# Kernel optimization log

Hardware: AMD Instinct MI355X
Metric: run time of the kernel (lower is better)

Reference implementation:

```python
import jax, jax.numpy as jnp
import numpy as np

B, N, E = 2, 30000, 120000
IN_F, OUT_F, H = 512, 512, 4
D = OUT_F // H  # head_dim = 128
LN_EPS = 1e-5


def setup_inputs() -> dict:
    key = jax.random.key(0)
    k1, k2, k3, k4 = jax.random.split(key, 4)
    node_features = jax.random.normal(k1, (B, N, IN_F), dtype=jnp.float32)
    edge_index = jax.random.randint(k2, (2, E), 0, N, dtype=jnp.int64)
    # per-head linear transforms (bias=False): W[h] is [in_features, head_dim]
    W = jax.random.normal(k3, (H, IN_F, D), dtype=jnp.float32) / np.sqrt(IN_F)
    # per-head attention vectors a[h] is [2*head_dim] (Linear(2*head_dim,1,bias=False))
    a = jax.random.normal(k4, (H, 2 * D), dtype=jnp.float32) / np.sqrt(2 * D)
    ln_gamma = jnp.ones((OUT_F,), dtype=jnp.float32)
    ln_beta = jnp.zeros((OUT_F,), dtype=jnp.float32)
    return {"node_features": node_features, "edge_index": edge_index,
            "W": W, "a": a, "ln_gamma": ln_gamma, "ln_beta": ln_beta}


def reference(node_features, edge_index, W, a, ln_gamma, ln_beta):
    src, dst = edge_index[0], edge_index[1]
    # all-heads linear transform: [B, H, N, D]
    t = jnp.einsum('bni,hid->bhnd', node_features, W)
    # per-edge gathered features: [B, H, E, D]
    sf = t[:, :, src, :]
    df = t[:, :, dst, :]
    # attention score = [sf ; df] . a  == sf.a_src + df.a_dst  -> [B, H, E]
    scores = (jnp.einsum('bhed,hd->bhe', sf, a[:, :D])
              + jnp.einsum('bhed,hd->bhe', df, a[:, D:]))
    scores = jax.nn.leaky_relu(scores, negative_slope=0.2)
    # NOTE: faithful to source — softmax over ALL edges (dim=-1), not per-dst
    w = jax.nn.softmax(scores, axis=-1)
    # scatter-add aggregation into destination nodes (the Python-loop in torch)
    agg = jnp.zeros_like(t).at[:, :, dst, :].add(w[..., None] * sf)  # [B,H,N,D]
    # concat heads along feature dim (head order preserved)
    out = jnp.transpose(agg, (0, 2, 1, 3)).reshape(node_features.shape[0], N, H * D)
    # LayerNorm over last dim
    mu = jnp.mean(out, axis=-1, keepdims=True)
    var = jnp.mean(jnp.square(out - mu), axis=-1, keepdims=True)
    out = (out - mu) * jax.lax.rsqrt(var + LN_EPS) * ln_gamma + ln_beta
    return out
```

## Files before the change

kernel.cpp:

```cpp
#include <hip/hip_runtime.h>
#include <stdint.h>

#define Bn 2
#define Nn 30000
#define En 120000
#define KIN 512
#define Hh 4
#define Dd 128
#define MROWS 60000
#define MPAD  60032
#define LNEPS 1e-5f
#define EBLK 469

typedef unsigned short u16;
typedef unsigned int   u32;
typedef __attribute__((ext_vector_type(8))) short short8;
typedef __attribute__((ext_vector_type(4))) float f32x4;

__device__ __forceinline__ u16 f2bf(float f) {
    u32 u = __builtin_bit_cast(u32, f);
    u32 r = u + 0x7FFFu + ((u >> 16) & 1u);
    return (u16)(r >> 16);
}
__device__ __forceinline__ float bflo(u32 u) {
    return __builtin_bit_cast(float, u << 16);
}
__device__ __forceinline__ float bfhi(u32 u) {
    return __builtin_bit_cast(float, u & 0xFFFF0000u);
}
__device__ __forceinline__ void ld16(void* lds, const void* g) {
    __builtin_amdgcn_global_load_lds((const __attribute__((address_space(1))) void*)g,
                                     (__attribute__((address_space(3))) void*)lds, 16, 0, 0);
}

#define CVTW_BLKS 1024
__global__ void prep_kernel(const float* __restrict__ W, u16* __restrict__ wbt,
                            const int* __restrict__ ei, int* __restrict__ deg) {
    int blk = blockIdx.x;
    if (blk < CVTW_BLKS) {
        int idx = blk * 256 + threadIdx.x;
        int c = idx >> 9, i = idx & 511;
        int h = c >> 7, d = c & 127;
        wbt[idx] = f2bf(W[h * (KIN * Dd) + i * Dd + d]);
    } else {
        int e = (blk - CVTW_BLKS) * 256 + threadIdx.x;
        if (e < En) atomicAdd(&deg[ei[En + e]], 1);
    }
}

__device__ void scan512(const int* __restrict__ deg, int* __restrict__ offs,
                        int* __restrict__ cursor, int* __restrict__ part) {
    int tid = threadIdx.x;
    const int CH = 59;
    int start = tid * CH;
    int s = 0;
    for (int i = 0; i < CH; i++) {
        int n = start + i;
        if (n < Nn) s += deg[n];
    }
    part[tid] = s;
    __syncthreads();
    for (int off = 1; off < 512; off <<= 1) {
        int xv = (tid >= off) ? part[tid - off] : 0;
        __syncthreads();
        part[tid] += xv;
        __syncthreads();
    }
    int run = part[tid] - s;
    for (int i = 0; i < CH; i++) {
        int n = start + i;
        if (n < Nn) {
            offs[n] = run;
            cursor[n] = run;
            run += deg[n];
        }
    }
    if (tid == 511) offs[Nn] = part[511];
}

#define A_LDS (2 * 128 * 32)
#define B_LDS (2 * 512 * 32)
__launch_bounds__(512)
__global__ void gemm(const float* __restrict__ x, const u16* __restrict__ wbt,
                     const float* __restrict__ ag, u16* __restrict__ t,
                     float* __restrict__ s1g, float* __restrict__ s2g,
                     const int* __restrict__ deg, int* __restrict__ offs,
                     int* __restrict__ cursor) {
    __shared__ __align__(16) u16 smem[A_LDS + B_LDS];
    if (blockIdx.x == 0) { scan512(deg, offs, cursor, (int*)smem); return; }
    u16* As0 = smem;
    u16* As1 = smem + 128 * 32;
    u16* Bs0 = smem + A_LDS;
    u16* Bs1 = smem + A_LDS + 512 * 32;
    const int tid = threadIdx.x;
    const int m0 = (blockIdx.x - 1) * 128;
    const int w = tid >> 6, l = tid & 63;
    const int lr = l & 15, lk = l >> 4;
    const int wrM = (w >> 2) * 64;
    const int h = w & 3;
    const int wc = h * 128;
    const int swz = (lk * 8) ^ ((lr & 6) << 2);
    int aoff[4], boff[8];
    #pragma unroll
    for (int mi = 0; mi < 4; mi++) aoff[mi] = (wrM + mi * 16 + lr) * 32 + swz;
    #pragma unroll
    for (int nj = 0; nj < 8; nj++) boff[nj] = (wc + nj * 16 + lr) * 32 + swz;

    const int arow_u = m0 + (tid >> 2);
    const int arow = arow_u < MROWS ? arow_u : (MROWS - 1);
    const float* xsrc = x + (long)arow * KIN + (tid & 3) * 8;
    const int awr = (tid >> 2) * 32 + (((tid & 3) * 8) ^ (((tid >> 2) & 6) << 2));

    const int grow = tid >> 2, gslot = tid & 3;
    const int gsw = (gslot * 8) ^ ((grow & 6) << 2);
    const u16* bgsrc = wbt + (long)grow * KIN + gsw;
    f32x4 acc[4][8] = {};
    float4 a0A, a1A, a0B, a1B;

#define LOADX(R0, R1, KS)                                           \
    {                                                               \
        R0 = *(const float4*)(xsrc + (KS) * 32);                    \
        R1 = *(const float4*)(xsrc + (KS) * 32 + 4);                \
    }
#define CVTW(BUF, R0, R1)                                           \
    {                                                               \
        short8 o;                                                   \
        o[0] = (short)f2bf(R0.x); o[1] = (short)f2bf(R0.y);         \
        o[2] = (short)f2bf(R0.z); o[3] = (short)f2bf(R0.w);         \
        o[4] = (short)f2bf(R1.x); o[5] = (short)f2bf(R1.y);         \
        o[6] = (short)f2bf(R1.z); o[7] = (short)f2bf(R1.w);         \
        *(short8*)&(BUF)[awr] = o;                                  \
    }

    auto STAGEB = [&](u16* Bb, int k0) {
        #pragma unroll
        for (int i = 0; i < 4; i++)
            ld16(Bb + ((long)(i * 512 + tid)) * 8, bgsrc + (long)i * 128 * KIN + k0);
    };

    LOADX(a0A, a1A, 0);
    LOADX(a0B, a1B, 1);
    STAGEB(Bs0, 0);
    CVTW(As0, a0A, a1A);
    __syncthreads();

    #pragma unroll
    for (int t16 = 0; t16 < 16; t16++) {
        u16* Acur = (t16 & 1) ? As1 : As0;
        u16* Bcur = (t16 & 1) ? Bs1 : Bs0;
        u16* Anext = (t16 & 1) ? As0 : As1;
        u16* Bnext = (t16 & 1) ? Bs0 : Bs1;
        if (t16 < 14) {
            if (t16 & 1) { LOADX(a0B, a1B, t16 + 2); }
            else         { LOADX(a0A, a1A, t16 + 2); }
        }
        if (t16 < 15) STAGEB(Bnext, (t16 + 1) * 32);
        short8 af[4];
        #pragma unroll
        for (int mi = 0; mi < 4; mi++) af[mi] = *(const short8*)&Acur[aoff[mi]];
        #pragma unroll
        for (int nj = 0; nj < 8; nj++) {
            short8 bv = *(const short8*)&Bcur[boff[nj]];
            #pragma unroll
            for (int mi = 0; mi < 4; mi++)
                acc[mi][nj] = __builtin_amdgcn_mfma_f32_16x16x32_bf16(
                    af[mi], bv, acc[mi][nj], 0, 0, 0);
        }
        if (t16 < 15) {
            if (t16 & 1) { CVTW(Anext, a0A, a1A); }
            else         { CVTW(Anext, a0B, a1B); }
        }
        __syncthreads();
    }
#undef LOADX
#undef CVTW

    #pragma unroll
    for (int mi = 0; mi < 4; mi++)
        #pragma unroll
        for (int r = 0; r < 4; r++) {
            int row = m0 + wrM + mi * 16 + lk * 4 + r;
            u16* tp = t + (long)row * 512 + wc + lr;
            #pragma unroll
            for (int nj = 0; nj < 8; nj++)
                tp[nj * 16] = f2bf(acc[mi][nj][r]);
        }
    float a1c[8], a2c[8];
    #pragma unroll
    for (int nj = 0; nj < 8; nj++) {
        int col = nj * 16 + lr;
        a1c[nj] = ag[h * 256 + col];
        a2c[nj] = ag[h * 256 + 128 + col];
    }
    float p1[16], p2[16];
    #pragma unroll
    for (int mi = 0; mi < 4; mi++)
        #pragma unroll
        for (int r = 0; r < 4; r++) {
            float v1 = 0.f, v2 = 0.f;
            #pragma unroll
            for (int nj = 0; nj < 8; nj++) {
                float tv = acc[mi][nj][r];
                v1 += tv * a1c[nj];
                v2 += tv * a2c[nj];
            }
            p1[mi * 4 + r] = v1;
            p2[mi * 4 + r] = v2;
        }
    #pragma unroll
    for (int off = 1; off < 16; off <<= 1)
        #pragma unroll
        for (int i = 0; i < 16; i++) {
            p1[i] += __shfl_xor(p1[i], off, 64);
            p2[i] += __shfl_xor(p2[i], off, 64);
        }
    if (lr == 0) {
        #pragma unroll
        for (int mi = 0; mi < 4; mi++)
            #pragma unroll
            for (int r = 0; r < 4; r++) {
                int row = m0 + wrM + mi * 16 + lk * 4 + r;
                if (row < MROWS) {
                    s1g[(long)row * 4 + h] = p1[mi * 4 + r];
                    s2g[(long)row * 4 + h] = p2[mi * 4 + r];
                }
            }
    }
}

__global__ void edgescatter_kernel(const int* __restrict__ ei, const float* __restrict__ s1,
                                   const float* __restrict__ s2, int* __restrict__ cursor,
                                   int* __restrict__ srcs, float* __restrict__ pw,
                                   float* __restrict__ Zpart) {
    int e = blockIdx.x * 256 + threadIdx.x;
    int tid = threadIdx.x;
    float v[8] = {0.f, 0.f, 0.f, 0.f, 0.f, 0.f, 0.f, 0.f};
    if (e < En) {
        int src = ei[e], dst = ei[En + e];
        #pragma unroll
        for (int b = 0; b < Bn; b++) {
            float4 v1 = *(const float4*)(s1 + ((long)b * Nn + src) * 4);
            float4 v2 = *(const float4*)(s2 + ((long)b * Nn + dst) * 4);
            float s;
            s = v1.x + v2.x; s = s > 0.f ? s : 0.2f * s; v[b * 4 + 0] = __expf(s);
            s = v1.y + v2.y; s = s > 0.f ? s : 0.2f * s; v[b * 4 + 1] = __expf(s);
            s = v1.z + v2.z; s = s > 0.f ? s : 0.2f * s; v[b * 4 + 2] = __expf(s);
            s = v1.w + v2.w; s = s > 0.f ? s : 0.2f * s; v[b * 4 + 3] = __expf(s);
        }
        int pos = atomicAdd(&cursor[dst], 1);
        srcs[pos] = src;
        *(float4*)(pw + (long)pos * 4)        = make_float4(v[0], v[1], v[2], v[3]);
        *(float4*)(pw + ((long)En + pos) * 4) = make_float4(v[4], v[5], v[6], v[7]);
    }
    #pragma unroll
    for (int off = 1; off < 64; off <<= 1)
        #pragma unroll
        for (int i = 0; i < 8; i++)
            v[i] += __shfl_xor(v[i], off, 64);
    __shared__ float red[4][8];
    if ((tid & 63) == 0)
        #pragma unroll
        for (int i = 0; i < 8; i++)
            red[tid >> 6][i] = v[i];
    __syncthreads();
    if (tid < 8)
        Zpart[(long)blockIdx.x * 8 + tid] =
            red[0][tid] + red[1][tid] + red[2][tid] + red[3][tid];
}

__global__ void zreduce_kernel(const float* __restrict__ Zpart, float* __restrict__ invZ) {
    int tid = threadIdx.x;
    int g = tid >> 5, l = tid & 31;
    float s = 0.f;
    for (int i = l; i < EBLK; i += 32)
        s += Zpart[(long)i * 8 + g];
    #pragma unroll
    for (int off = 1; off < 32; off <<= 1)
        s += __shfl_xor(s, off, 64);
    if (l == 0) invZ[g] = 1.0f / s;
}

__launch_bounds__(128)
__global__ void agg_kernel(const u16* __restrict__ t, const int* __restrict__ srcs,
                           const float* __restrict__ pw, const float* __restrict__ invZ,
                           const int* __restrict__ offs,
                           const float* __restrict__ gamma, const float* __restrict__ beta,
                           float* __restrict__ out) {
    int tid = threadIdx.x;
    int b = tid >> 6;
    int l = tid & 63;
    int n = blockIdx.x;
    int h = l >> 4;
    int j0 = offs[n], j1 = offs[n + 1];
    const float* pwb = pw + (long)b * En * 4;
    const u16* tb = t + (long)b * Nn * 512;
    float a0 = 0.f, a1 = 0.f, a2 = 0.f, a3 = 0.f;
    float a4 = 0.f, a5 = 0.f, a6 = 0.f, a7 = 0.f;
    for (int j = j0; j < j1; j += 4) {
        int  jj0 = j,     jj1 = j + 1,  jj2 = j + 2,  jj3 = j + 3;
        bool k1 = jj1 < j1, k2 = jj2 < j1, k3 = jj3 < j1;
        int  i1 = k1 ? jj1 : j0, i2 = k2 ? jj2 : j0, i3 = k3 ? jj3 : j0;
        int s0 = srcs[jj0], s1i = srcs[i1], s2i = srcs[i2], s3i = srcs[i3];
        float w0 = pwb[(long)jj0 * 4 + h];
        float w1 = k1 ? pwb[(long)i1 * 4 + h] : 0.f;
        float w2 = k2 ? pwb[(long)i2 * 4 + h] : 0.f;
        float w3 = k3 ? pwb[(long)i3 * 4 + h] : 0.f;
        uint4 r0 = *(const uint4*)(tb + (long)s0 * 512 + l * 8);
        uint4 r1 = *(const uint4*)(tb + (long)s1i * 512 + l * 8);
        uint4 r2 = *(const uint4*)(tb + (long)s2i * 512 + l * 8);
        uint4 r3 = *(const uint4*)(tb + (long)s3i * 512 + l * 8);
        a0 += w0 * bflo(r0.x) + w1 * bflo(r1.x) + w2 * bflo(r2.x) + w3 * bflo(r3.x);
        a1 += w0 * bfhi(r0.x) + w1 * bfhi(r1.x) + w2 * bfhi(r2.x) + w3 * bfhi(r3.x);
        a2 += w0 * bflo(r0.y) + w1 * bflo(r1.y) + w2 * bflo(r2.y) + w3 * bflo(r3.y);
        a3 += w0 * bfhi(r0.y) + w1 * bfhi(r1.y) + w2 * bfhi(r2.y) + w3 * bfhi(r3.y);
        a4 += w0 * bflo(r0.z) + w1 * bflo(r1.z) + w2 * bflo(r2.z) + w3 * bflo(r3.z);
        a5 += w0 * bfhi(r0.z) + w1 * bfhi(r1.z) + w2 * bfhi(r2.z) + w3 * bfhi(r3.z);
        a6 += w0 * bflo(r0.w) + w1 * bflo(r1.w) + w2 * bflo(r2.w) + w3 * bflo(r3.w);
        a7 += w0 * bfhi(r0.w) + w1 * bfhi(r1.w) + w2 * bfhi(r2.w) + w3 * bfhi(r3.w);
    }
    float invz = invZ[b * 4 + h];
    a0 *= invz; a1 *= invz; a2 *= invz; a3 *= invz;
    a4 *= invz; a5 *= invz; a6 *= invz; a7 *= invz;
    float s  = a0 + a1 + a2 + a3 + a4 + a5 + a6 + a7;
    float ss = a0 * a0 + a1 * a1 + a2 * a2 + a3 * a3
             + a4 * a4 + a5 * a5 + a6 * a6 + a7 * a7;
    #pragma unroll
    for (int off = 1; off < 64; off <<= 1) {
        s  += __shfl_xor(s, off, 64);
        ss += __shfl_xor(ss, off, 64);
    }
    float mean = s * (1.0f / 512.0f);
    float var = ss * (1.0f / 512.0f) - mean * mean;
    var = var < 0.f ? 0.f : var;
    float scale = rsqrtf(var + LNEPS);
    int c = l * 8;
    float4 g0 = *(const float4*)(gamma + c);
    float4 g1 = *(const float4*)(gamma + c + 4);
    float4 b0 = *(const float4*)(beta + c);
    float4 b1 = *(const float4*)(beta + c + 4);
    float4 o0, o1;
    o0.x = (a0 - mean) * scale * g0.x + b0.x;
    o0.y = (a1 - mean) * scale * g0.y + b0.y;
    o0.z = (a2 - mean) * scale * g0.z + b0.z;
    o0.w = (a3 - mean) * scale * g0.w + b0.w;
    o1.x = (a4 - mean) * scale * g1.x + b1.x;
    o1.y = (a5 - mean) * scale * g1.y + b1.y;
    o1.z = (a6 - mean) * scale * g1.z + b1.z;
    o1.w = (a7 - mean) * scale * g1.w + b1.w;
    float* op = out + ((long)b * Nn + n) * 512 + c;
    *(float4*)(op)     = o0;
    *(float4*)(op + 4) = o1;
}

extern "C" void kernel_launch(void* const* d_in, const int* in_sizes, int n_in,
                              void* d_out, int out_size, void* d_ws, size_t ws_size,
                              hipStream_t stream) {
    const float* x     = (const float*)d_in[0];
    const int*   ei    = (const int*)d_in[1];
    const float* W     = (const float*)d_in[2];
    const float* a     = (const float*)d_in[3];
    const float* gamma = (const float*)d_in[4];
    const float* beta  = (const float*)d_in[5];
    float* out = (float*)d_out;

    char* ws = (char*)d_ws;
    size_t off = 0;
    auto alloc = [&](size_t bytes) -> void* {
        void* ptr = ws + off;
        off = (off + bytes + 255) & ~(size_t)255;
        return ptr;
    };
    u16*   wbt    = (u16*)alloc((size_t)512 * 512 * 2);
    u16*   t      = (u16*)alloc((size_t)MPAD * 512 * 2);
    float* s1     = (float*)alloc((size_t)MROWS * 4 * 4);
    float* s2     = (float*)alloc((size_t)MROWS * 4 * 4);
    float* pw     = (float*)alloc((size_t)Bn * En * 4 * 4);
    float* Zpart  = (float*)alloc((size_t)EBLK * 8 * 4);
    float* invZ   = (float*)alloc(8 * 4);
    int*   deg    = (int*)alloc((size_t)Nn * 4);
    int*   offs   = (int*)alloc((size_t)(Nn + 1) * 4);
    int*   cursor = (int*)alloc((size_t)Nn * 4);
    int*   srcs   = (int*)alloc((size_t)En * 4);

    hipMemsetAsync(deg, 0, (size_t)Nn * 4, stream);

    prep_kernel<<<CVTW_BLKS + EBLK, 256, 0, stream>>>(W, wbt, ei, deg);
    gemm<<<470, 512, 0, stream>>>(x, wbt, a, t, s1, s2, deg, offs, cursor);
    edgescatter_kernel<<<EBLK, 256, 0, stream>>>(ei, s1, s2, cursor, srcs, pw, Zpart);
    zreduce_kernel<<<1, 256, 0, stream>>>(Zpart, invZ);
    agg_kernel<<<Nn, 128, 0, stream>>>(t, srcs, pw, invZ, offs, gamma, beta, out);
}
```

Measured before the change: 361.7 us.

## Halve GEMM M-tile to 64 rows and fold Z reduction into atomics

The GEMM block tile shrinks from 128 to 64 rows, so each of the 8 waves now covers a 64x64 output slice. The grid doubles to 939 blocks, with a launch-bounds occupancy hint and LDS-based combining of the per-head score partials across wave pairs. This aims at better CU occupancy and load balance on a 256-CU part, at the cost of reloading the B operand (W) twice as often. Separately, the zreduce kernel launch is removed: edge blocks atomically add their partial softmax denominators into an 8-float buffer that is zeroed by a memset, and the aggregation kernel computes the reciprocal itself.

```diff
diff --git a/kernel.cpp b/kernel.cpp
--- a/kernel.cpp
+++ b/kernel.cpp
@@ -15,6 +15,7 @@
 typedef unsigned short u16;
 typedef unsigned int   u32;
 typedef __attribute__((ext_vector_type(8))) short short8;
+typedef __attribute__((ext_vector_type(4))) short bf16x4;
 typedef __attribute__((ext_vector_type(4))) float f32x4;
 
 __device__ __forceinline__ u16 f2bf(float f) {
@@ -78,58 +79,51 @@
     if (tid == 511) offs[Nn] = part[511];
 }
 
-#define A_LDS (2 * 128 * 32)
-#define B_LDS (2 * 512 * 32)
-__launch_bounds__(512)
+#define A_LDSU 4096
+#define B_LDSU 32768
+__launch_bounds__(512, 4)
 __global__ void gemm(const float* __restrict__ x, const u16* __restrict__ wbt,
                      const float* __restrict__ ag, u16* __restrict__ t,
                      float* __restrict__ s1g, float* __restrict__ s2g,
                      const int* __restrict__ deg, int* __restrict__ offs,
                      int* __restrict__ cursor) {
-    __shared__ __align__(16) u16 smem[A_LDS + B_LDS];
+    __shared__ __align__(16) u16 smem[A_LDSU + B_LDSU];
     if (blockIdx.x == 0) { scan512(deg, offs, cursor, (int*)smem); return; }
     u16* As0 = smem;
-    u16* As1 = smem + 128 * 32;
-    u16* Bs0 = smem + A_LDS;
-    u16* Bs1 = smem + A_LDS + 512 * 32;
+    u16* As1 = smem + 2048;
+    u16* Bs0 = smem + A_LDSU;
+    u16* Bs1 = smem + A_LDSU + 16384;
     const int tid = threadIdx.x;
-    const int m0 = (blockIdx.x - 1) * 128;
+    const int m0 = (blockIdx.x - 1) * 64;
     const int w = tid >> 6, l = tid & 63;
     const int lr = l & 15, lk = l >> 4;
-    const int wrM = (w >> 2) * 64;
-    const int h = w & 3;
-    const int wc = h * 128;
+    const int h = w >> 1;
+    const int wc = w * 64;
     const int swz = (lk * 8) ^ ((lr & 6) << 2);
-    int aoff[4], boff[8];
-    #pragma unroll
-    for (int mi = 0; mi < 4; mi++) aoff[mi] = (wrM + mi * 16 + lr) * 32 + swz;
-    #pragma unroll
-    for (int nj = 0; nj < 8; nj++) boff[nj] = (wc + nj * 16 + lr) * 32 + swz;
-
-    const int arow_u = m0 + (tid >> 2);
+    int aoff[4], boff[4];
+    #pragma unroll
+    for (int mi = 0; mi < 4; mi++) aoff[mi] = (mi * 16 + lr) * 32 + swz;
+    #pragma unroll
+    for (int nj = 0; nj < 4; nj++) boff[nj] = (wc + nj * 16 + lr) * 32 + swz;
+
+    const int arow_u = m0 + (tid >> 3);
     const int arow = arow_u < MROWS ? arow_u : (MROWS - 1);
-    const float* xsrc = x + (long)arow * KIN + (tid & 3) * 8;
-    const int awr = (tid >> 2) * 32 + (((tid & 3) * 8) ^ (((tid >> 2) & 6) << 2));
+    const float* xsrc = x + (long)arow * KIN + (tid & 7) * 4;
+    const int awr = (tid >> 3) * 32 + (((tid & 7) * 4) ^ (((tid >> 3) & 6) << 2));
 
     const int grow = tid >> 2, gslot = tid & 3;
     const int gsw = (gslot * 8) ^ ((grow & 6) << 2);
     const u16* bgsrc = wbt + (long)grow * KIN + gsw;
-    f32x4 acc[4][8] = {};
-    float4 a0A, a1A, a0B, a1B;
-
-#define LOADX(R0, R1, KS)                                           \
+    f32x4 acc[4][4] = {};
+    float4 rxA, rxB;
+
+#define LOADX(R, KS)  { R = *(const float4*)(xsrc + (KS) * 32); }
+#define CVTW(BUF, R)                                                \
     {                                                               \
-        R0 = *(const float4*)(xsrc + (KS) * 32);                    \
-        R1 = *(const float4*)(xsrc + (KS) * 32 + 4);                \
-    }
-#define CVTW(BUF, R0, R1)                                           \
-    {                                                               \
-        short8 o;                                                   \
-        o[0] = (short)f2bf(R0.x); o[1] = (short)f2bf(R0.y);         \
-        o[2] = (short)f2bf(R0.z); o[3] = (short)f2bf(R0.w);         \
-        o[4] = (short)f2bf(R1.x); o[5] = (short)f2bf(R1.y);         \
-        o[6] = (short)f2bf(R1.z); o[7] = (short)f2bf(R1.w);         \
-        *(short8*)&(BUF)[awr] = o;                                  \
+        bf16x4 o;                                                   \
+        o[0] = (short)f2bf(R.x); o[1] = (short)f2bf(R.y);           \
+        o[2] = (short)f2bf(R.z); o[3] = (short)f2bf(R.w);           \
+        *(bf16x4*)&(BUF)[awr] = o;                                  \
     }
 
     auto STAGEB = [&](u16* Bb, int k0) {
@@ -138,10 +132,10 @@
             ld16(Bb + ((long)(i * 512 + tid)) * 8, bgsrc + (long)i * 128 * KIN + k0);
     };
 
-    LOADX(a0A, a1A, 0);
-    LOADX(a0B, a1B, 1);
+    LOADX(rxA, 0);
+    LOADX(rxB, 1);
     STAGEB(Bs0, 0);
-    CVTW(As0, a0A, a1A);
+    CVTW(As0, rxA);
     __syncthreads();
 
     #pragma unroll
@@ -151,15 +145,15 @@
         u16* Anext = (t16 & 1) ? As0 : As1;
         u16* Bnext = (t16 & 1) ? Bs0 : Bs1;
         if (t16 < 14) {
-            if (t16 & 1) { LOADX(a0B, a1B, t16 + 2); }
-            else         { LOADX(a0A, a1A, t16 + 2); }
+            if (t16 & 1) { LOADX(rxB, t16 + 2); }
+            else         { LOADX(rxA, t16 + 2); }
         }
         if (t16 < 15) STAGEB(Bnext, (t16 + 1) * 32);
         short8 af[4];
         #pragma unroll
         for (int mi = 0; mi < 4; mi++) af[mi] = *(const short8*)&Acur[aoff[mi]];
         #pragma unroll
-        for (int nj = 0; nj < 8; nj++) {
+        for (int nj = 0; nj < 4; nj++) {
             short8 bv = *(const short8*)&Bcur[boff[nj]];
             #pragma unroll
             for (int mi = 0; mi < 4; mi++)
@@ -167,8 +161,8 @@
                     af[mi], bv, acc[mi][nj], 0, 0, 0);
         }
         if (t16 < 15) {
-            if (t16 & 1) { CVTW(Anext, a0A, a1A); }
-            else         { CVTW(Anext, a0B, a1B); }
+            if (t16 & 1) { CVTW(Anext, rxA); }
+            else         { CVTW(Anext, rxB); }
         }
         __syncthreads();
     }
@@ -179,16 +173,16 @@
     for (int mi = 0; mi < 4; mi++)
         #pragma unroll
         for (int r = 0; r < 4; r++) {
-            int row = m0 + wrM + mi * 16 + lk * 4 + r;
+            int row = m0 + mi * 16 + lk * 4 + r;
             u16* tp = t + (long)row * 512 + wc + lr;
             #pragma unroll
-            for (int nj = 0; nj < 8; nj++)
+            for (int nj = 0; nj < 4; nj++)
                 tp[nj * 16] = f2bf(acc[mi][nj][r]);
         }
-    float a1c[8], a2c[8];
-    #pragma unroll
-    for (int nj = 0; nj < 8; nj++) {
-        int col = nj * 16 + lr;
+    float a1c[4], a2c[4];
+    #pragma unroll
+    for (int nj = 0; nj < 4; nj++) {
+        int col = (w & 1) * 64 + nj * 16 + lr;
         a1c[nj] = ag[h * 256 + col];
         a2c[nj] = ag[h * 256 + 128 + col];
     }
@@ -199,7 +193,7 @@
         for (int r = 0; r < 4; r++) {
             float v1 = 0.f, v2 = 0.f;
             #pragma unroll
-            for (int nj = 0; nj < 8; nj++) {
+            for (int nj = 0; nj < 4; nj++) {
                 float tv = acc[mi][nj][r];
                 v1 += tv * a1c[nj];
                 v2 += tv * a2c[nj];
@@ -214,24 +208,35 @@
             p1[i] += __shfl_xor(p1[i], off, 64);
             p2[i] += __shfl_xor(p2[i], off, 64);
         }
+    float* S = (float*)smem;
     if (lr == 0) {
         #pragma unroll
         for (int mi = 0; mi < 4; mi++)
             #pragma unroll
             for (int r = 0; r < 4; r++) {
-                int row = m0 + wrM + mi * 16 + lk * 4 + r;
-                if (row < MROWS) {
-                    s1g[(long)row * 4 + h] = p1[mi * 4 + r];
-                    s2g[(long)row * 4 + h] = p2[mi * 4 + r];
-                }
+                int row = mi * 16 + lk * 4 + r;
+                S[0 * 512 + w * 64 + row] = p1[mi * 4 + r];
+                S[1 * 512 + w * 64 + row] = p2[mi * 4 + r];
             }
+    }
+    __syncthreads();
+    {
+        int si = tid >> 8;
+        int rem = tid & 255;
+        int hh = rem >> 6, row = rem & 63;
+        int grw = m0 + row;
+        if (grw < MROWS) {
+            float v = S[si * 512 + (hh * 2) * 64 + row]
+                    + S[si * 512 + (hh * 2 + 1) * 64 + row];
+            (si ? s2g : s1g)[(long)grw * 4 + hh] = v;
+        }
     }
 }
 
 __global__ void edgescatter_kernel(const int* __restrict__ ei, const float* __restrict__ s1,
                                    const float* __restrict__ s2, int* __restrict__ cursor,
                                    int* __restrict__ srcs, float* __restrict__ pw,
-                                   float* __restrict__ Zpart) {
+                                   float* __restrict__ Zsum) {
     int e = blockIdx.x * 256 + threadIdx.x;
     int tid = threadIdx.x;
     float v[8] = {0.f, 0.f, 0.f, 0.f, 0.f, 0.f, 0.f, 0.f};
@@ -264,25 +269,12 @@
             red[tid >> 6][i] = v[i];
     __syncthreads();
     if (tid < 8)
-        Zpart[(long)blockIdx.x * 8 + tid] =
-            red[0][tid] + red[1][tid] + red[2][tid] + red[3][tid];
-}
-
-__global__ void zreduce_kernel(const float* __restrict__ Zpart, float* __restrict__ invZ) {
-    int tid = threadIdx.x;
-    int g = tid >> 5, l = tid & 31;
-    float s = 0.f;
-    for (int i = l; i < EBLK; i += 32)
-        s += Zpart[(long)i * 8 + g];
-    #pragma unroll
-    for (int off = 1; off < 32; off <<= 1)
-        s += __shfl_xor(s, off, 64);
-    if (l == 0) invZ[g] = 1.0f / s;
+        atomicAdd(&Zsum[tid], red[0][tid] + red[1][tid] + red[2][tid] + red[3][tid]);
 }
 
 __launch_bounds__(128)
 __global__ void agg_kernel(const u16* __restrict__ t, const int* __restrict__ srcs,
-                           const float* __restrict__ pw, const float* __restrict__ invZ,
+                           const float* __restrict__ pw, const float* __restrict__ Zsum,
                            const int* __restrict__ offs,
                            const float* __restrict__ gamma, const float* __restrict__ beta,
                            float* __restrict__ out) {
@@ -318,7 +310,7 @@
         a6 += w0 * bflo(r0.w) + w1 * bflo(r1.w) + w2 * bflo(r2.w) + w3 * bflo(r3.w);
         a7 += w0 * bfhi(r0.w) + w1 * bfhi(r1.w) + w2 * bfhi(r2.w) + w3 * bfhi(r3.w);
     }
-    float invz = invZ[b * 4 + h];
+    float invz = 1.0f / Zsum[b * 4 + h];
     a0 *= invz; a1 *= invz; a2 *= invz; a3 *= invz;
     a4 *= invz; a5 *= invz; a6 *= invz; a7 *= invz;
     float s  = a0 + a1 + a2 + a3 + a4 + a5 + a6 + a7;
@@ -375,18 +367,17 @@
     float* s1     = (float*)alloc((size_t)MROWS * 4 * 4);
     float* s2     = (float*)alloc((size_t)MROWS * 4 * 4);
     float* pw     = (float*)alloc((size_t)Bn * En * 4 * 4);
-    float* Zpart  = (float*)alloc((size_t)EBLK * 8 * 4);
-    float* invZ   = (float*)alloc(8 * 4);
+    float* Zsum   = (float*)alloc(8 * 4);
     int*   deg    = (int*)alloc((size_t)Nn * 4);
     int*   offs   = (int*)alloc((size_t)(Nn + 1) * 4);
     int*   cursor = (int*)alloc((size_t)Nn * 4);
     int*   srcs   = (int*)alloc((size_t)En * 4);
 
     hipMemsetAsync(deg, 0, (size_t)Nn * 4, stream);
+    hipMemsetAsync(Zsum, 0, 8 * 4, stream);
 
     prep_kernel<<<CVTW_BLKS + EBLK, 256, 0, stream>>>(W, wbt, ei, deg);
-    gemm<<<470, 512, 0, stream>>>(x, wbt, a, t, s1, s2, deg, offs, cursor);
-    edgescatter_kernel<<<EBLK, 256, 0, stream>>>(ei, s1, s2, cursor, srcs, pw, Zpart);
-    zreduce_kernel<<<1, 256, 0, stream>>>(Zpart, invZ);
-    agg_kernel<<<Nn, 128, 0, stream>>>(t, srcs, pw, invZ, offs, gamma, beta, out);
-}
+    gemm<<<939, 512, 0, stream>>>(x, wbt, a, t, s1, s2, deg, offs, cursor);
+    edgescatter_kernel<<<EBLK, 256, 0, stream>>>(ei, s1, s2, cursor, srcs, pw, Zsum);
+    agg_kernel<<<Nn, 128, 0, stream>>>(t, srcs, pw, Zsum, offs, gamma, beta, out);
+}
```

Result: slower. 375.4 us (+3.8%).

## Transpose MFMA output, stage GEMM epilogue through LDS, fold Z reduction into atomics

Applied to the files above, without the earlier changes.

The MFMA operands are swapped so each lane holds four consecutive columns. This allows a cheaper attention-score dot product with vector loads of the a vector and fewer shuffles. The GEMM epilogue now writes the bf16 tile into LDS and stores it to global memory as coalesced 16-byte rows instead of scattered 2-byte stores. The separate zreduce kernel is replaced by per-block atomicAdds into a zeroed Zsum, which removes one launch but makes the float summation order nondeterministic.

```diff
diff --git a/kernel.cpp b/kernel.cpp
--- a/kernel.cpp
+++ b/kernel.cpp
@@ -15,6 +15,7 @@
 typedef unsigned short u16;
 typedef unsigned int   u32;
 typedef __attribute__((ext_vector_type(8))) short short8;
+typedef __attribute__((ext_vector_type(4))) short bf16x4;
 typedef __attribute__((ext_vector_type(4))) float f32x4;
 
 __device__ __forceinline__ u16 f2bf(float f) {
@@ -164,7 +165,7 @@
             #pragma unroll
             for (int mi = 0; mi < 4; mi++)
                 acc[mi][nj] = __builtin_amdgcn_mfma_f32_16x16x32_bf16(
-                    af[mi], bv, acc[mi][nj], 0, 0, 0);
+                    bv, af[mi], acc[mi][nj], 0, 0, 0);
         }
         if (t16 < 15) {
             if (t16 & 1) { CVTW(Anext, a0A, a1A); }
@@ -175,63 +176,68 @@
 #undef LOADX
 #undef CVTW
 
-    #pragma unroll
-    for (int mi = 0; mi < 4; mi++)
-        #pragma unroll
-        for (int r = 0; r < 4; r++) {
-            int row = m0 + wrM + mi * 16 + lk * 4 + r;
-            u16* tp = t + (long)row * 512 + wc + lr;
+    float p1[4] = {0.f, 0.f, 0.f, 0.f}, p2[4] = {0.f, 0.f, 0.f, 0.f};
+    #pragma unroll
+    for (int nj = 0; nj < 8; nj++) {
+        float4 c1 = *(const float4*)(ag + h * 256 + nj * 16 + lk * 4);
+        float4 c2 = *(const float4*)(ag + h * 256 + 128 + nj * 16 + lk * 4);
+        #pragma unroll
+        for (int mi = 0; mi < 4; mi++) {
+            p1[mi] += acc[mi][nj][0] * c1.x + acc[mi][nj][1] * c1.y
+                    + acc[mi][nj][2] * c1.z + acc[mi][nj][3] * c1.w;
+            p2[mi] += acc[mi][nj][0] * c2.x + acc[mi][nj][1] * c2.y
+                    + acc[mi][nj][2] * c2.z + acc[mi][nj][3] * c2.w;
+        }
+    }
+    #pragma unroll
+    for (int off = 16; off < 64; off <<= 1)
+        #pragma unroll
+        for (int mi = 0; mi < 4; mi++) {
+            p1[mi] += __shfl_xor(p1[mi], off, 64);
+            p2[mi] += __shfl_xor(p2[mi], off, 64);
+        }
+    if (lk == 0) {
+        #pragma unroll
+        for (int mi = 0; mi < 4; mi++) {
+            int row = m0 + wrM + mi * 16 + lr;
+            if (row < MROWS) {
+                s1g[(long)row * 4 + h] = p1[mi];
+                s2g[(long)row * 4 + h] = p2[mi];
+            }
+        }
+    }
+
+    {
+        u16* T = smem + w * 5120;
+        const int l8 = l & 7, li = l >> 3;
+        #pragma unroll
+        for (int h2 = 0; h2 < 2; h2++) {
             #pragma unroll
-            for (int nj = 0; nj < 8; nj++)
-                tp[nj * 16] = f2bf(acc[mi][nj][r]);
-        }
-    float a1c[8], a2c[8];
-    #pragma unroll
-    for (int nj = 0; nj < 8; nj++) {
-        int col = nj * 16 + lr;
-        a1c[nj] = ag[h * 256 + col];
-        a2c[nj] = ag[h * 256 + 128 + col];
-    }
-    float p1[16], p2[16];
-    #pragma unroll
-    for (int mi = 0; mi < 4; mi++)
-        #pragma unroll
-        for (int r = 0; r < 4; r++) {
-            float v1 = 0.f, v2 = 0.f;
+            for (int mi = 0; mi < 4; mi++)
+                #pragma unroll
+                for (int nj4 = 0; nj4 < 4; nj4++) {
+                    int nj = h2 * 4 + nj4;
+                    bf16x4 o;
+                    o[0] = (short)f2bf(acc[mi][nj][0]);
+                    o[1] = (short)f2bf(acc[mi][nj][1]);
+                    o[2] = (short)f2bf(acc[mi][nj][2]);
+                    o[3] = (short)f2bf(acc[mi][nj][3]);
+                    *(bf16x4*)&T[(mi * 16 + lr) * 80 + nj4 * 16 + lk * 4] = o;
+                }
             #pragma unroll
-            for (int nj = 0; nj < 8; nj++) {
-                float tv = acc[mi][nj][r];
-                v1 += tv * a1c[nj];
-                v2 += tv * a2c[nj];
+            for (int i = 0; i < 8; i++) {
+                int rowL = i * 8 + li;
+                short8 v = *(const short8*)&T[rowL * 80 + l8 * 8];
+                *(short8*)(t + (long)(m0 + wrM + rowL) * 512 + wc + h2 * 64 + l8 * 8) = v;
             }
-            p1[mi * 4 + r] = v1;
-            p2[mi * 4 + r] = v2;
-        }
-    #pragma unroll
-    for (int off = 1; off < 16; off <<= 1)
-        #pragma unroll
-        for (int i = 0; i < 16; i++) {
-            p1[i] += __shfl_xor(p1[i], off, 64);
-            p2[i] += __shfl_xor(p2[i], off, 64);
-        }
-    if (lr == 0) {
-        #pragma unroll
-        for (int mi = 0; mi < 4; mi++)
-            #pragma unroll
-            for (int r = 0; r < 4; r++) {
-                int row = m0 + wrM + mi * 16 + lk * 4 + r;
-                if (row < MROWS) {
-                    s1g[(long)row * 4 + h] = p1[mi * 4 + r];
-                    s2g[(long)row * 4 + h] = p2[mi * 4 + r];
-                }
-            }
+        }
     }
 }
 
 __global__ void edgescatter_kernel(const int* __restrict__ ei, const float* __restrict__ s1,
                                    const float* __restrict__ s2, int* __restrict__ cursor,
                                    int* __restrict__ srcs, float* __restrict__ pw,
-                                   float* __restrict__ Zpart) {
+                                   float* __restrict__ Zsum) {
     int e = blockIdx.x * 256 + threadIdx.x;
     int tid = threadIdx.x;
     float v[8] = {0.f, 0.f, 0.f, 0.f, 0.f, 0.f, 0.f, 0.f};
@@ -264,25 +270,12 @@
             red[tid >> 6][i] = v[i];
     __syncthreads();
     if (tid < 8)
-        Zpart[(long)blockIdx.x * 8 + tid] =
-            red[0][tid] + red[1][tid] + red[2][tid] + red[3][tid];
-}
-
-__global__ void zreduce_kernel(const float* __restrict__ Zpart, float* __restrict__ invZ) {
-    int tid = threadIdx.x;
-    int g = tid >> 5, l = tid & 31;
-    float s = 0.f;
-    for (int i = l; i < EBLK; i += 32)
-        s += Zpart[(long)i * 8 + g];
-    #pragma unroll
-    for (int off = 1; off < 32; off <<= 1)
-        s += __shfl_xor(s, off, 64);
-    if (l == 0) invZ[g] = 1.0f / s;
+        atomicAdd(&Zsum[tid], red[0][tid] + red[1][tid] + red[2][tid] + red[3][tid]);
 }
 
 __launch_bounds__(128)
 __global__ void agg_kernel(const u16* __restrict__ t, const int* __restrict__ srcs,
-                           const float* __restrict__ pw, const float* __restrict__ invZ,
+                           const float* __restrict__ pw, const float* __restrict__ Zsum,
                            const int* __restrict__ offs,
                            const float* __restrict__ gamma, const float* __restrict__ beta,
                            float* __restrict__ out) {
@@ -299,7 +292,7 @@
     for (int j = j0; j < j1; j += 4) {
         int  jj0 = j,     jj1 = j + 1,  jj2 = j + 2,  jj3 = j + 3;
         bool k1 = jj1 < j1, k2 = jj2 < j1, k3 = jj3 < j1;
-        int  i1 = k1 ? jj1 : j0, i2 = k2 ? jj2 : j0, i3 = k3 ? jj3 : j0;
+        int  i1 = k1 ? jj1 : jj0, i2 = k2 ? jj2 : jj0, i3 = k3 ? jj3 : jj0;
         int s0 = srcs[jj0], s1i = srcs[i1], s2i = srcs[i2], s3i = srcs[i3];
         float w0 = pwb[(long)jj0 * 4 + h];
         float w1 = k1 ? pwb[(long)i1 * 4 + h] : 0.f;
@@ -318,7 +311,7 @@
         a6 += w0 * bflo(r0.w) + w1 * bflo(r1.w) + w2 * bflo(r2.w) + w3 * bflo(r3.w);
         a7 += w0 * bfhi(r0.w) + w1 * bfhi(r1.w) + w2 * bfhi(r2.w) + w3 * bfhi(r3.w);
     }
-    float invz = invZ[b * 4 + h];
+    float invz = 1.0f / Zsum[b * 4 + h];
     a0 *= invz; a1 *= invz; a2 *= invz; a3 *= invz;
     a4 *= invz; a5 *= invz; a6 *= invz; a7 *= invz;
     float s  = a0 + a1 + a2 + a3 + a4 + a5 + a6 + a7;
@@ -375,18 +368,17 @@
     float* s1     = (float*)alloc((size_t)MROWS * 4 * 4);
     float* s2     = (float*)alloc((size_t)MROWS * 4 * 4);
     float* pw     = (float*)alloc((size_t)Bn * En * 4 * 4);
-    float* Zpart  = (float*)alloc((size_t)EBLK * 8 * 4);
-    float* invZ   = (float*)alloc(8 * 4);
+    float* Zsum   = (float*)alloc(8 * 4);
     int*   deg    = (int*)alloc((size_t)Nn * 4);
     int*   offs   = (int*)alloc((size_t)(Nn + 1) * 4);
     int*   cursor = (int*)alloc((size_t)Nn * 4);
     int*   srcs   = (int*)alloc((size_t)En * 4);
 
     hipMemsetAsync(deg, 0, (size_t)Nn * 4, stream);
+    hipMemsetAsync(Zsum, 0, 8 * 4, stream);
 
     prep_kernel<<<CVTW_BLKS + EBLK, 256, 0, stream>>>(W, wbt, ei, deg);
     gemm<<<470, 512, 0, stream>>>(x, wbt, a, t, s1, s2, deg, offs, cursor);
-    edgescatter_kernel<<<EBLK, 256, 0, stream>>>(ei, s1, s2, cursor, srcs, pw, Zpart);
-    zreduce_kernel<<<1, 256, 0, stream>>>(Zpart, invZ);
-    agg_kernel<<<Nn, 128, 0, stream>>>(t, srcs, pw, invZ, offs, gamma, beta, out);
-}
+    edgescatter_kernel<<<EBLK, 256, 0, stream>>>(ei, s1, s2, cursor, srcs, pw, Zsum);
+    agg_kernel<<<Nn, 128, 0, stream>>>(t, srcs, pw, Zsum, offs, gamma, beta, out);
+}
```

New measurement: 359.8 us. About the same (-0.5%).
